# Performance work log

Hardware: AMD Instinct MI355X
Metric: run time of the kernel (lower is better)

Reference implementation:

```python
import jax, jax.numpy as jnp
import numpy as np

EPS = 1e-5


def setup_inputs() -> dict:
    key = jax.random.key(0)
    k_x, k_y, k_w, k_b = jax.random.split(key, 4)
    B, IN, OUT = 16384, 1024, 1024
    x = jax.random.normal(k_x, (B, IN), dtype=jnp.float32)
    y = jax.random.normal(k_y, (B, OUT), dtype=jnp.float32)
    # nn.Linear default init scale ~ 1/sqrt(in_features); keep activations sane
    weight = jax.random.normal(k_w, (OUT, IN), dtype=jnp.float32) / np.sqrt(IN)
    bias = jax.random.normal(k_b, (OUT,), dtype=jnp.float32) / np.sqrt(IN)
    gamma = jnp.ones((OUT,), dtype=jnp.float32)
    beta = jnp.zeros((OUT,), dtype=jnp.float32)
    return {"x": x, "y": y, "weight": weight, "bias": bias, "gamma": gamma, "beta": beta}


def reference(x, y, weight, bias, gamma, beta):
    # Linear: z[b, o] = sum_i x[b, i] * weight[o, i] + bias[o]
    z = jnp.einsum('bi,oi->bo', x, weight) + bias
    # LayerNorm over the feature (out_features) dim, biased variance
    mean = jnp.mean(z, axis=-1, keepdims=True)
    var = jnp.mean(jnp.square(z), axis=-1, keepdims=True) - jnp.square(mean)
    ln = (z - mean) * jax.lax.rsqrt(var + EPS) * gamma + beta
    # residual add then elementwise multiply
    return (ln + y) * y
```

## Files before the change

kernel.cpp:

```cpp
#include <hip/hip_runtime.h>
#include <stdint.h>

typedef unsigned short u16;
typedef __attribute__((ext_vector_type(8))) short short8;
typedef __attribute__((ext_vector_type(4))) float floatx4;
typedef __attribute__((ext_vector_type(2))) float floatx2;

#define K_DIM 1024
#define N_DIM 1024
#define BM 64
#define BK 32
#define NCHUNK (K_DIM / BK)
#define HCHUNK (NCHUNK / 2)

__device__ __forceinline__ u16 f2b(float f) {
    union { float f; uint32_t i; } v; v.f = f;
    uint32_t u = v.i;
    return (u16)((u + 0x7FFFu + ((u >> 16) & 1u)) >> 16);
}
__device__ __forceinline__ float b2f(u16 u) {
    union { uint32_t i; float f; } v; v.i = ((uint32_t)u) << 16; return v.f;
}

__global__ __launch_bounds__(256) void pack_w_kernel(const float* __restrict__ w,
                                                     u16* __restrict__ wpk) {
    int gid  = blockIdx.x * 256 + threadIdx.x;
    int lane = gid & 63;
    int kc   = (gid >> 6) & 31;
    int tile = gid >> 11;
    int n = tile * 16 + (lane & 15);
    int k = kc * 32 + (lane >> 4) * 8;
    const float* src = w + (size_t)n * K_DIM + k;
    floatx4 a = *(const floatx4*)(src);
    floatx4 b = *(const floatx4*)(src + 4);
    short8 o;
    o[0] = (short)f2b(a[0]); o[1] = (short)f2b(a[1]);
    o[2] = (short)f2b(a[2]); o[3] = (short)f2b(a[3]);
    o[4] = (short)f2b(b[0]); o[5] = (short)f2b(b[1]);
    o[6] = (short)f2b(b[2]); o[7] = (short)f2b(b[3]);
    *(short8*)(wpk + (size_t)gid * 8) = o;
}

__global__ __launch_bounds__(1024) void fused_gemm_ln_kernel(
    const float* __restrict__ x, const float* __restrict__ y,
    const u16* __restrict__ wpk, const float* __restrict__ bias,
    const float* __restrict__ gamma, const float* __restrict__ beta,
    float* __restrict__ out)
{
    __shared__ __align__(16) u16 lds16[HCHUNK * BM * BK];
    __shared__ __align__(16) u16 zbuf[16 * 1024];
    __shared__ float ls_sum[64];
    __shared__ float ls_sum2[64];
    __shared__ float ls_mean[64];
    __shared__ float ls_rs[64];

    const int tid  = threadIdx.x;
    const int lane = tid & 63;
    const int wv   = tid >> 6;
    const int q    = lane >> 4;
    const int row0 = blockIdx.x * BM;

    if (tid < 64) { ls_sum[tid] = 0.0f; ls_sum2[tid] = 0.0f; }

    const int sr = tid >> 4;
    const int sk = (tid & 15) << 1;
    const float* s_src = x + (size_t)(row0 + sr) * K_DIM + sk;
    const int s_qs  = (sk >> 3) ^ ((sr >> 1) & 3);
    const int s_off = sr * 64 + s_qs * 16 + (sk & 7) * 2;

    const u16* bp = wpk + (size_t)wv * 65536 + lane * 8;

    const int a_base = (lane & 15) * 64 + (q ^ (((lane & 15) >> 1) & 3)) * 16;

    floatx4 acc[4][4];
#pragma unroll
    for (int mi = 0; mi < 4; ++mi)
#pragma unroll
        for (int ni = 0; ni < 4; ++ni)
            acc[mi][ni] = (floatx4){0.0f, 0.0f, 0.0f, 0.0f};

#pragma unroll 4
    for (int c = 0; c < HCHUNK; ++c) {
        floatx2 v = *(const floatx2*)(s_src + c * BK);
        uint32_t p = (uint32_t)f2b(v[0]) | ((uint32_t)f2b(v[1]) << 16);
        *(uint32_t*)((char*)lds16 + c * 4096 + s_off) = p;
    }

    short8 bfr[2][4];
#pragma unroll
    for (int ni = 0; ni < 4; ++ni)
        bfr[0][ni] = *(const short8*)(bp + ni * 16384);

    __syncthreads();

    for (int half = 0; half < 2; ++half) {
        if (half == 1) {
            __syncthreads();
#pragma unroll 4
            for (int c = 0; c < HCHUNK; ++c) {
                floatx2 v = *(const floatx2*)(s_src + (HCHUNK + c) * BK);
                uint32_t p = (uint32_t)f2b(v[0]) | ((uint32_t)f2b(v[1]) << 16);
                *(uint32_t*)((char*)lds16 + c * 4096 + s_off) = p;
            }
            __syncthreads();
        }

#pragma unroll 2
        for (int c = 0; c < HCHUNK; ++c) {
            const int kc  = half * HCHUNK + c;
            const int cur = kc & 1;
            const int nxt = cur ^ 1;
            const char* ab = (const char*)lds16 + c * 4096;

            short8 af0 = *(const short8*)(ab + a_base);
            short8 af1 = *(const short8*)(ab + a_base + 1024);
            short8 af2 = *(const short8*)(ab + a_base + 2048);
            short8 af3 = *(const short8*)(ab + a_base + 3072);

            const int kn = (kc + 1 < NCHUNK) ? (kc + 1) : kc;
#pragma unroll
            for (int ni = 0; ni < 4; ++ni)
                bfr[nxt][ni] = *(const short8*)(bp + ni * 16384 + kn * 512);

#pragma unroll
            for (int ni = 0; ni < 4; ++ni) {
                acc[0][ni] = __builtin_amdgcn_mfma_f32_16x16x32_bf16(
                    af0, bfr[cur][ni], acc[0][ni], 0, 0, 0);
                acc[1][ni] = __builtin_amdgcn_mfma_f32_16x16x32_bf16(
                    af1, bfr[cur][ni], acc[1][ni], 0, 0, 0);
                acc[2][ni] = __builtin_amdgcn_mfma_f32_16x16x32_bf16(
                    af2, bfr[cur][ni], acc[2][ni], 0, 0, 0);
                acc[3][ni] = __builtin_amdgcn_mfma_f32_16x16x32_bf16(
                    af3, bfr[cur][ni], acc[3][ni], 0, 0, 0);
            }
        }
    }

    float bias_v[4];
#pragma unroll
    for (int ni = 0; ni < 4; ++ni)
        bias_v[ni] = bias[(wv << 6) + (ni << 4) + (lane & 15)];
#pragma unroll
    for (int mi = 0; mi < 4; ++mi)
#pragma unroll
        for (int ni = 0; ni < 4; ++ni)
#pragma unroll
            for (int r = 0; r < 4; ++r)
                acc[mi][ni][r] += bias_v[ni];

    __syncthreads();

#pragma unroll
    for (int mi = 0; mi < 4; ++mi)
#pragma unroll
        for (int r = 0; r < 4; ++r) {
            float s = 0.0f, s2 = 0.0f;
#pragma unroll
            for (int ni = 0; ni < 4; ++ni) {
                float v = acc[mi][ni][r];
                s += v; s2 += v * v;
            }
#pragma unroll
            for (int m = 1; m < 16; m <<= 1) {
                s  += __shfl_xor(s,  m, 64);
                s2 += __shfl_xor(s2, m, 64);
            }
            if ((lane & 15) == 0) {
                int rl = (mi << 4) + (q << 2) + r;
                atomicAdd(&ls_sum[rl], s);
                atomicAdd(&ls_sum2[rl], s2);
            }
        }

    __syncthreads();
    if (tid < 64) {
        float mean = ls_sum[tid] * (1.0f / 1024.0f);
        float var  = ls_sum2[tid] * (1.0f / 1024.0f) - mean * mean;
        ls_mean[tid] = mean;
        ls_rs[tid]   = rsqrtf(var + 1e-5f);
    }

    for (int mi = 0; mi < 4; ++mi) {
#pragma unroll
        for (int ni = 0; ni < 4; ++ni)
#pragma unroll
            for (int r = 0; r < 4; ++r) {
                int lr   = (q << 2) + r;
                int lin  = (((wv << 6) + (ni << 4) + (lane & 15)) << 1);
                int phys = lr * 2048 + (lin ^ (q << 5));
                *(u16*)((char*)zbuf + phys) = f2b(acc[mi][ni][r]);
            }
        __syncthreads();
#pragma unroll
        for (int it = 0; it < 2; ++it) {
            int row  = (tid >> 7) + (it << 3);
            int c8   = tid & 127;
            int phys = row * 2048 + ((c8 << 4) ^ (((row >> 2) & 3) << 5));
            short8 z8 = *(const short8*)((const char*)zbuf + phys);
            int grow  = row0 + (mi << 4) + row;
            float mean = ls_mean[(mi << 4) + row];
            float rs   = ls_rs[(mi << 4) + row];
            const float* yp = y     + (size_t)grow * N_DIM + c8 * 8;
            const float* gp = gamma + c8 * 8;
            const float* bpv = beta + c8 * 8;
            float*       op = out   + (size_t)grow * N_DIM + c8 * 8;
            floatx4 y0 = *(const floatx4*)(yp);
            floatx4 y1 = *(const floatx4*)(yp + 4);
            floatx4 g0 = *(const floatx4*)(gp);
            floatx4 g1 = *(const floatx4*)(gp + 4);
            floatx4 b0 = *(const floatx4*)(bpv);
            floatx4 b1 = *(const floatx4*)(bpv + 4);
            floatx4 o0, o1;
#pragma unroll
            for (int e = 0; e < 4; ++e) {
                float zv = b2f((u16)z8[e]);
                o0[e] = ((zv - mean) * rs * g0[e] + b0[e] + y0[e]) * y0[e];
            }
#pragma unroll
            for (int e = 0; e < 4; ++e) {
                float zv = b2f((u16)z8[e + 4]);
                o1[e] = ((zv - mean) * rs * g1[e] + b1[e] + y1[e]) * y1[e];
            }
            *(floatx4*)(op)     = o0;
            *(floatx4*)(op + 4) = o1;
        }
        __syncthreads();
    }
}

extern "C" void kernel_launch(void* const* d_in, const int* in_sizes, int n_in,
                              void* d_out, int out_size, void* d_ws, size_t ws_size,
                              hipStream_t stream) {
    const float* x     = (const float*)d_in[0];
    const float* y     = (const float*)d_in[1];
    const float* wgt   = (const float*)d_in[2];
    const float* bias  = (const float*)d_in[3];
    const float* gamma = (const float*)d_in[4];
    const float* beta  = (const float*)d_in[5];
    float* out = (float*)d_out;
    u16* wpk = (u16*)d_ws;

    pack_w_kernel<<<512, 256, 0, stream>>>(wgt, wpk);

    const int M = in_sizes[0] / K_DIM;
    fused_gemm_ln_kernel<<<M / BM, 1024, 0, stream>>>(x, y, wpk, bias, gamma, beta, out);
}
```

Before: 216.9 us.

## Split fused GEMM+LayerNorm into GEMM-with-stats and separate LN apply kernel

Splits the fused kernel in two when workspace allows. The first kernel does the GEMM, computes per-row mean and rsqrt, and writes z as bf16 to workspace. A separate elementwise kernel then reads z, y, gamma and beta to produce the output. The goal is to take the y loads and the epilogue out of the 1024-thread GEMM blocks, which have low occupancy, and run them in a kernel that parallelises better. The cost is an extra 32 MB bf16 round-trip through global memory plus one more kernel launch.

Result: slower. 225.6 us (+4.0%).

```diff
diff --git a/kernel.cpp b/kernel.cpp
--- a/kernel.cpp
+++ b/kernel.cpp
@@ -41,6 +41,202 @@
     *(short8*)(wpk + (size_t)gid * 8) = o;
 }
 
+__global__ __launch_bounds__(1024) void gemm_stats_kernel(
+    const float* __restrict__ x, const u16* __restrict__ wpk,
+    const float* __restrict__ bias, u16* __restrict__ zout,
+    float* __restrict__ stats)
+{
+    __shared__ __align__(16) u16 lds16[HCHUNK * BM * BK];
+    __shared__ __align__(16) u16 zbuf[16 * 1024];
+    __shared__ float ls_sum[64];
+    __shared__ float ls_sum2[64];
+
+    const int tid  = threadIdx.x;
+    const int lane = tid & 63;
+    const int wv   = tid >> 6;
+    const int q    = lane >> 4;
+    const int row0 = blockIdx.x * BM;
+
+    if (tid < 64) { ls_sum[tid] = 0.0f; ls_sum2[tid] = 0.0f; }
+
+    const int sr = tid >> 4;
+    const int sk = (tid & 15) << 1;
+    const float* s_src = x + (size_t)(row0 + sr) * K_DIM + sk;
+    const int s_qs  = (sk >> 3) ^ ((sr >> 1) & 3);
+    const int s_off = sr * 64 + s_qs * 16 + (sk & 7) * 2;
+
+    const u16* bp = wpk + (size_t)wv * 65536 + lane * 8;
+
+    const int a_base = (lane & 15) * 64 + (q ^ (((lane & 15) >> 1) & 3)) * 16;
+
+    floatx4 acc[4][4];
+#pragma unroll
+    for (int mi = 0; mi < 4; ++mi)
+#pragma unroll
+        for (int ni = 0; ni < 4; ++ni)
+            acc[mi][ni] = (floatx4){0.0f, 0.0f, 0.0f, 0.0f};
+
+#pragma unroll 4
+    for (int c = 0; c < HCHUNK; ++c) {
+        floatx2 v = *(const floatx2*)(s_src + c * BK);
+        uint32_t p = (uint32_t)f2b(v[0]) | ((uint32_t)f2b(v[1]) << 16);
+        *(uint32_t*)((char*)lds16 + c * 4096 + s_off) = p;
+    }
+
+    short8 bfr[2][4];
+#pragma unroll
+    for (int ni = 0; ni < 4; ++ni)
+        bfr[0][ni] = *(const short8*)(bp + ni * 16384);
+
+    __syncthreads();
+
+    for (int half = 0; half < 2; ++half) {
+        if (half == 1) {
+            __syncthreads();
+#pragma unroll 4
+            for (int c = 0; c < HCHUNK; ++c) {
+                floatx2 v = *(const floatx2*)(s_src + (HCHUNK + c) * BK);
+                uint32_t p = (uint32_t)f2b(v[0]) | ((uint32_t)f2b(v[1]) << 16);
+                *(uint32_t*)((char*)lds16 + c * 4096 + s_off) = p;
+            }
+            __syncthreads();
+        }
+
+#pragma unroll 2
+        for (int c = 0; c < HCHUNK; ++c) {
+            const int kc  = half * HCHUNK + c;
+            const int cur = kc & 1;
+            const int nxt = cur ^ 1;
+            const char* ab = (const char*)lds16 + c * 4096;
+
+            short8 af0 = *(const short8*)(ab + a_base);
+            short8 af1 = *(const short8*)(ab + a_base + 1024);
+            short8 af2 = *(const short8*)(ab + a_base + 2048);
+            short8 af3 = *(const short8*)(ab + a_base + 3072);
+
+            const int kn = (kc + 1 < NCHUNK) ? (kc + 1) : kc;
+#pragma unroll
+            for (int ni = 0; ni < 4; ++ni)
+                bfr[nxt][ni] = *(const short8*)(bp + ni * 16384 + kn * 512);
+
+#pragma unroll
+            for (int ni = 0; ni < 4; ++ni) {
+                acc[0][ni] = __builtin_amdgcn_mfma_f32_16x16x32_bf16(
+                    af0, bfr[cur][ni], acc[0][ni], 0, 0, 0);
+                acc[1][ni] = __builtin_amdgcn_mfma_f32_16x16x32_bf16(
+                    af1, bfr[cur][ni], acc[1][ni], 0, 0, 0);
+                acc[2][ni] = __builtin_amdgcn_mfma_f32_16x16x32_bf16(
+                    af2, bfr[cur][ni], acc[2][ni], 0, 0, 0);
+                acc[3][ni] = __builtin_amdgcn_mfma_f32_16x16x32_bf16(
+                    af3, bfr[cur][ni], acc[3][ni], 0, 0, 0);
+            }
+        }
+    }
+
+    float bias_v[4];
+#pragma unroll
+    for (int ni = 0; ni < 4; ++ni)
+        bias_v[ni] = bias[(wv << 6) + (ni << 4) + (lane & 15)];
+#pragma unroll
+    for (int mi = 0; mi < 4; ++mi)
+#pragma unroll
+        for (int ni = 0; ni < 4; ++ni)
+#pragma unroll
+            for (int r = 0; r < 4; ++r)
+                acc[mi][ni][r] += bias_v[ni];
+
+    __syncthreads();
+
+#pragma unroll
+    for (int mi = 0; mi < 4; ++mi)
+#pragma unroll
+        for (int r = 0; r < 4; ++r) {
+            float s = 0.0f, s2 = 0.0f;
+#pragma unroll
+            for (int ni = 0; ni < 4; ++ni) {
+                float v = acc[mi][ni][r];
+                s += v; s2 += v * v;
+            }
+#pragma unroll
+            for (int m = 1; m < 16; m <<= 1) {
+                s  += __shfl_xor(s,  m, 64);
+                s2 += __shfl_xor(s2, m, 64);
+            }
+            if ((lane & 15) == 0) {
+                int rl = (mi << 4) + (q << 2) + r;
+                atomicAdd(&ls_sum[rl], s);
+                atomicAdd(&ls_sum2[rl], s2);
+            }
+        }
+
+    __syncthreads();
+    if (tid < 64) {
+        float mean = ls_sum[tid] * (1.0f / 1024.0f);
+        float var  = ls_sum2[tid] * (1.0f / 1024.0f) - mean * mean;
+        stats[row0 + tid]           = mean;
+        stats[16384 + row0 + tid]   = rsqrtf(var + 1e-5f);
+    }
+
+    for (int mi = 0; mi < 4; ++mi) {
+#pragma unroll
+        for (int ni = 0; ni < 4; ++ni)
+#pragma unroll
+            for (int r = 0; r < 4; ++r) {
+                int lr   = (q << 2) + r;
+                int lin  = (((wv << 6) + (ni << 4) + (lane & 15)) << 1);
+                int phys = lr * 2048 + (lin ^ (q << 5));
+                *(u16*)((char*)zbuf + phys) = f2b(acc[mi][ni][r]);
+            }
+        __syncthreads();
+#pragma unroll
+        for (int it = 0; it < 2; ++it) {
+            int row  = (tid >> 7) + (it << 3);
+            int c8   = tid & 127;
+            int phys = row * 2048 + ((c8 << 4) ^ (((row >> 2) & 3) << 5));
+            short8 z8 = *(const short8*)((const char*)zbuf + phys);
+            int grow  = row0 + (mi << 4) + row;
+            *(short8*)(zout + (size_t)grow * N_DIM + c8 * 8) = z8;
+        }
+        __syncthreads();
+    }
+}
+
+__global__ __launch_bounds__(256) void ln_apply_kernel(
+    const u16* __restrict__ z, const float* __restrict__ y,
+    const float* __restrict__ stats, const float* __restrict__ gamma,
+    const float* __restrict__ beta, float* __restrict__ out)
+{
+    int g   = blockIdx.x * 256 + threadIdx.x;
+    int row = g >> 7;
+    int c8  = g & 127;
+    float mean = stats[row];
+    float rs   = stats[16384 + row];
+    short8 z8 = *(const short8*)(z + (size_t)row * N_DIM + c8 * 8);
+    const float* yp  = y     + (size_t)row * N_DIM + c8 * 8;
+    const float* gp  = gamma + c8 * 8;
+    const float* bpv = beta  + c8 * 8;
+    float*       op  = out   + (size_t)row * N_DIM + c8 * 8;
+    floatx4 y0 = *(const floatx4*)(yp);
+    floatx4 y1 = *(const floatx4*)(yp + 4);
+    floatx4 g0 = *(const floatx4*)(gp);
+    floatx4 g1 = *(const floatx4*)(gp + 4);
+    floatx4 b0 = *(const floatx4*)(bpv);
+    floatx4 b1 = *(const floatx4*)(bpv + 4);
+    floatx4 o0, o1;
+#pragma unroll
+    for (int e = 0; e < 4; ++e) {
+        float zv = b2f((u16)z8[e]);
+        o0[e] = ((zv - mean) * rs * g0[e] + b0[e] + y0[e]) * y0[e];
+    }
+#pragma unroll
+    for (int e = 0; e < 4; ++e) {
+        float zv = b2f((u16)z8[e + 4]);
+        o1[e] = ((zv - mean) * rs * g1[e] + b1[e] + y1[e]) * y1[e];
+    }
+    *(floatx4*)(op)     = o0;
+    *(floatx4*)(op + 4) = o1;
+}
+
 __global__ __launch_bounds__(1024) void fused_gemm_ln_kernel(
     const float* __restrict__ x, const float* __restrict__ y,
     const u16* __restrict__ wpk, const float* __restrict__ bias,
@@ -69,7 +265,6 @@
     const int s_off = sr * 64 + s_qs * 16 + (sk & 7) * 2;
 
     const u16* bp = wpk + (size_t)wv * 65536 + lane * 8;
-
     const int a_base = (lane & 15) * 64 + (q ^ (((lane & 15) >> 1) & 3)) * 16;
 
     floatx4 acc[4][4];
@@ -85,12 +280,10 @@
         uint32_t p = (uint32_t)f2b(v[0]) | ((uint32_t)f2b(v[1]) << 16);
         *(uint32_t*)((char*)lds16 + c * 4096 + s_off) = p;
     }
-
     short8 bfr[2][4];
 #pragma unroll
     for (int ni = 0; ni < 4; ++ni)
         bfr[0][ni] = *(const short8*)(bp + ni * 16384);
-
     __syncthreads();
 
     for (int half = 0; half < 2; ++half) {
@@ -104,24 +297,20 @@
             }
             __syncthreads();
         }
-
 #pragma unroll 2
         for (int c = 0; c < HCHUNK; ++c) {
             const int kc  = half * HCHUNK + c;
             const int cur = kc & 1;
             const int nxt = cur ^ 1;
             const char* ab = (const char*)lds16 + c * 4096;
-
             short8 af0 = *(const short8*)(ab + a_base);
             short8 af1 = *(const short8*)(ab + a_base + 1024);
             short8 af2 = *(const short8*)(ab + a_base + 2048);
             short8 af3 = *(const short8*)(ab + a_base + 3072);
-
             const int kn = (kc + 1 < NCHUNK) ? (kc + 1) : kc;
 #pragma unroll
             for (int ni = 0; ni < 4; ++ni)
                 bfr[nxt][ni] = *(const short8*)(bp + ni * 16384 + kn * 512);
-
 #pragma unroll
             for (int ni = 0; ni < 4; ++ni) {
                 acc[0][ni] = __builtin_amdgcn_mfma_f32_16x16x32_bf16(
@@ -238,10 +427,23 @@
     const float* gamma = (const float*)d_in[4];
     const float* beta  = (const float*)d_in[5];
     float* out = (float*)d_out;
+
     u16* wpk = (u16*)d_ws;
+    const size_t WPK_BYTES   = 2u * 1024u * 1024u;
+    const size_t STATS_BYTES = 128u * 1024u;
+    const size_t Z_BYTES     = 32u * 1024u * 1024u;
+    const int M = in_sizes[0] / K_DIM;
 
     pack_w_kernel<<<512, 256, 0, stream>>>(wgt, wpk);
 
-    const int M = in_sizes[0] / K_DIM;
-    fused_gemm_ln_kernel<<<M / BM, 1024, 0, stream>>>(x, y, wpk, bias, gamma, beta, out);
-}
+    if (ws_size >= WPK_BYTES + STATS_BYTES + Z_BYTES) {
+        float* stats = (float*)((char*)d_ws + WPK_BYTES);
+        u16*   zws   = (u16*)((char*)d_ws + WPK_BYTES + STATS_BYTES);
+        gemm_stats_kernel<<<M / BM, 1024, 0, stream>>>(x, wpk, bias, zws, stats);
+        ln_apply_kernel<<<M * (N_DIM / 8) / 256, 256, 0, stream>>>(
+            zws, y, stats, gamma, beta, out);
+    } else {
+        fused_gemm_ln_kernel<<<M / BM, 1024, 0, stream>>>(
+            x, y, wpk, bias, gamma, beta, out);
+    }
+}
```
